# Kernel tuning notes

Hardware: AMD Instinct MI355X
Metric: run time of the kernel (lower is better)

Reference implementation:

```python
import jax, jax.numpy as jnp
import numpy as np

B, S, HID = 2, 2048, 2048
H, KVH, D = 32, 8, 64          # query heads, kv heads, head_dim
G = H // KVH                    # GQA group size (num_key_value_groups)
ROT = 32                        # head_dim * partial_rotary_factor
THETA = 10000.0
NEG = -1e9


def setup_inputs() -> dict:
    key = jax.random.key(0)
    ks = jax.random.split(key, 5)
    hidden_states = jax.random.normal(ks[0], (B, S, HID), jnp.float32) * 0.02
    Wq = jax.random.normal(ks[1], (H * D, HID), jnp.float32) * 0.02
    Wk = jax.random.normal(ks[2], (KVH * D, HID), jnp.float32) * 0.02
    Wv = jax.random.normal(ks[3], (KVH * D, HID), jnp.float32) * 0.02
    Wo = jax.random.normal(ks[4], (HID, H * D), jnp.float32) * 0.02
    # rotary embeddings over the partial rotary dims
    inv_freq = 1.0 / (THETA ** (jnp.arange(0, ROT, 2, dtype=jnp.float32) / ROT))
    freqs = jnp.arange(S, dtype=jnp.float32)[:, None] * inv_freq[None, :]  # [S, ROT/2]
    emb = jnp.concatenate([freqs, freqs], axis=-1)                         # [S, ROT]
    cos = jnp.broadcast_to(jnp.cos(emb)[None], (B, S, ROT)).astype(jnp.float32)
    sin = jnp.broadcast_to(jnp.sin(emb)[None], (B, S, ROT)).astype(jnp.float32)
    # HF-style additive causal mask [1, 1, S, S]
    causal = jnp.tril(jnp.ones((S, S), dtype=bool))
    attention_mask = jnp.where(causal, 0.0, NEG).astype(jnp.float32)[None, None]
    return {"hidden_states": hidden_states, "cos": cos, "sin": sin,
            "attention_mask": attention_mask, "Wq": Wq, "Wk": Wk, "Wv": Wv, "Wo": Wo}


def _rotate_half(x):
    half = x.shape[-1] // 2
    return jnp.concatenate([-x[..., half:], x[..., :half]], axis=-1)


def _apply_partial_rope(x, cos, sin):
    # x: [B, h, S, D]; cos/sin: [B, 1, S, ROT]
    xr, xp = x[..., :ROT], x[..., ROT:]
    xr = xr * cos + _rotate_half(xr) * sin
    return jnp.concatenate([xr, xp], axis=-1)


def reference(hidden_states, cos, sin, attention_mask, Wq, Wk, Wv, Wo):
    bsz, q_len, _ = hidden_states.shape
    q = (hidden_states @ Wq.T).reshape(bsz, q_len, H, D).transpose(0, 2, 1, 3)    # [B,H,S,D]
    k = (hidden_states @ Wk.T).reshape(bsz, q_len, KVH, D).transpose(0, 2, 1, 3)  # [B,KVH,S,D]
    v = (hidden_states @ Wv.T).reshape(bsz, q_len, KVH, D).transpose(0, 2, 1, 3)
    cos_e, sin_e = cos[:, None], sin[:, None]  # unsqueeze_dim=1
    q = _apply_partial_rope(q, cos_e, sin_e)
    k = _apply_partial_rope(k, cos_e, sin_e)
    # GQA: group q heads instead of materializing repeat_kv (same math)
    qg = q.reshape(bsz, KVH, G, q_len, D)
    scores = jnp.einsum('bkgsd,bktd->bkgst', qg, k) / jnp.sqrt(jnp.float32(D))
    scores = scores + attention_mask[:, :, None, :, :q_len]  # [B,KVH,G,S,S]
    attn = jax.nn.softmax(scores.astype(jnp.float32), axis=-1).astype(q.dtype)
    out = jnp.einsum('bkgst,bktd->bkgsd', attn, v)
    out = out.reshape(bsz, H, q_len, D).transpose(0, 2, 1, 3).reshape(bsz, q_len, H * D)
    return out @ Wo.T
```

## Files before the change

### kernel.cpp

```cpp
#include <hip/hip_runtime.h>
#include <hip/hip_bf16.h>

#define BATCH 2
#define SEQ 2048
#define HID 2048
#define NH 32
#define NKVH 8
#define HD 64
#define GQ 4
#define ROT 32

typedef __attribute__((ext_vector_type(8))) short bf16x8;
typedef __attribute__((ext_vector_type(8))) unsigned short u16x8;
typedef __attribute__((ext_vector_type(4))) float f32x4;
typedef unsigned int u32;
typedef unsigned short u16;

#define MFMA_BF16(A, B, C) __builtin_amdgcn_mfma_f32_16x16x32_bf16(A, B, C, 0, 0, 0)

#define QSCALE 0.180336880111120f

__device__ __forceinline__ void gload_lds16(const void* g, void* l) {
    __builtin_amdgcn_global_load_lds(
        (const __attribute__((address_space(1))) unsigned int*)g,
        (__attribute__((address_space(3))) unsigned int*)l, 16, 0, 0);
}

__device__ __forceinline__ u16 f2b(float x) {
    union { __hip_bfloat16 h; u16 u; } cv;
    cv.h = __float2bfloat16(x);
    return cv.u;
}
__device__ __forceinline__ u32 pack2r(float lo, float hi) {
    u32 a = __builtin_bit_cast(u32, lo) + 0x8000u;
    u32 b = __builtin_bit_cast(u32, hi) + 0x8000u;
    return __builtin_amdgcn_perm(b, a, 0x07060302u);
}

__global__ __launch_bounds__(256) void cast_all(
    const float* __restrict__ hs, const float* __restrict__ Wq,
    const float* __restrict__ Wk, const float* __restrict__ Wv,
    const float* __restrict__ Wo, u16* __restrict__ d_hs, u16* __restrict__ d_Wq,
    u16* __restrict__ d_Wk, u16* __restrict__ d_Wv, u16* __restrict__ d_Wo) {
    const int bx = blockIdx.x;
    const float* s;
    u16* d;
    int off;
    if (bx < 4096) { s = hs; d = d_hs; off = bx; }
    else if (bx < 6144) { s = Wq; d = d_Wq; off = bx - 4096; }
    else if (bx < 6656) { s = Wk; d = d_Wk; off = bx - 6144; }
    else if (bx < 7168) { s = Wv; d = d_Wv; off = bx - 6656; }
    else { s = Wo; d = d_Wo; off = bx - 7168; }
    const size_t i = (size_t)off * 2048 + threadIdx.x * 8;
    const float4 a = *(const float4*)&s[i];
    const float4 b = *(const float4*)&s[i + 4];
    u16x8 v;
    v[0] = f2b(a.x); v[1] = f2b(a.y); v[2] = f2b(a.z); v[3] = f2b(a.w);
    v[4] = f2b(b.x); v[5] = f2b(b.y); v[6] = f2b(b.z); v[7] = f2b(b.w);
    *(u16x8*)&d[i] = v;
}

__global__ __launch_bounds__(256) void qkv_gemm(
    const u16* __restrict__ A, const u16* __restrict__ Wq,
    const u16* __restrict__ Wk, const u16* __restrict__ Wv,
    u16* __restrict__ Qb, u16* __restrict__ Kb, u16* __restrict__ Vt,
    const float* __restrict__ cosp, const float* __restrict__ sinp) {
    const int bid = blockIdx.x;
    const int xcd = bid & 7, loc = bid >> 3;
    const int x = xcd * 3 + (loc % 3);
    const int m0 = (loc / 3) * 128;

    int mode, n0;
    const u16* __restrict__ W;
    if (x < 16)      { mode = 0; W = Wq; n0 = x * 128; }
    else if (x < 20) { mode = 1; W = Wk; n0 = (x - 16) * 128; }
    else             { mode = 2; W = Wv; n0 = (x - 20) * 128; }

    __shared__ __align__(16) u16 As[128 * 64];
    __shared__ __align__(16) u16 Ws[128 * 64];
    const int tid = threadIdx.x;
    const int lane = tid & 63, wave = tid >> 6;
    const int ar = lane & 15, quad = lane >> 4;
    const int q4 = quad * 4;
    const int wm = (wave >> 1) * 64, wn = (wave & 1) * 64;

    f32x4 acc[4][4] = {};

    for (int k0 = 0; k0 < HID; k0 += 64) {
#pragma unroll
        for (int it = 0; it < 4; ++it) {
            const int ci = it * 256 + tid;
            const int row = ci >> 3, kcl = ci & 7;
            const int kcg = kcl ^ (row & 7);
            gload_lds16(&A[(size_t)(m0 + row) * HID + k0 + kcg * 8], &As[ci * 8]);
            gload_lds16(&W[(size_t)(n0 + row) * HID + k0 + kcg * 8], &Ws[ci * 8]);
        }
        __syncthreads();
#pragma unroll
        for (int kh = 0; kh < 2; ++kh) {
            bf16x8 af[4], bf[4];
#pragma unroll
            for (int t = 0; t < 4; ++t) {
                const int ra = wm + t * 16 + ar;
                af[t] = *(const bf16x8*)&As[ra * 64 + (((kh * 4 + quad) ^ (ra & 7))) * 8];
                const int rb = wn + t * 16 + ar;
                bf[t] = *(const bf16x8*)&Ws[rb * 64 + (((kh * 4 + quad) ^ (rb & 7))) * 8];
            }
            if (mode < 2) {
#pragma unroll
                for (int mt = 0; mt < 4; ++mt)
#pragma unroll
                    for (int nt = 0; nt < 4; ++nt)
                        acc[mt][nt] = MFMA_BF16(bf[nt], af[mt], acc[mt][nt]);
            } else {
#pragma unroll
                for (int mt = 0; mt < 4; ++mt)
#pragma unroll
                    for (int nt = 0; nt < 4; ++nt)
                        acc[mt][nt] = MFMA_BF16(af[mt], bf[nt], acc[mt][nt]);
            }
        }
        __syncthreads();
    }

    if (mode < 2) {
        const float SC = (mode == 0) ? QSCALE : 1.0f;
        u16* __restrict__ C = (mode == 0) ? Qb : Kb;
        const int N = (mode == 0) ? 2048 : 512;
#pragma unroll
        for (int mt = 0; mt < 4; ++mt) {
            const int t = m0 + wm + mt * 16 + ar;
            const float4 c0 = *(const float4*)&cosp[(size_t)t * ROT + q4];
            const float4 s0 = *(const float4*)&sinp[(size_t)t * ROT + q4];
            const float4 c1 = *(const float4*)&cosp[(size_t)t * ROT + 16 + q4];
            const float4 s1 = *(const float4*)&sinp[(size_t)t * ROT + 16 + q4];
            u16* crow = &C[(size_t)t * N + n0 + wn];
            const f32x4 x0 = acc[mt][0], x1 = acc[mt][1];
            const float cr0[4] = {c0.x, c0.y, c0.z, c0.w};
            const float sr0[4] = {s0.x, s0.y, s0.z, s0.w};
            const float cr1[4] = {c1.x, c1.y, c1.z, c1.w};
            const float sr1[4] = {s1.x, s1.y, s1.z, s1.w};
            float o0[4], o1[4];
#pragma unroll
            for (int r = 0; r < 4; ++r) {
                o0[r] = (x0[r] * cr0[r] - x1[r] * sr0[r]) * SC;
                o1[r] = (x1[r] * cr1[r] + x0[r] * sr1[r]) * SC;
            }
            uint2 v;
            v.x = pack2r(o0[0], o0[1]); v.y = pack2r(o0[2], o0[3]);
            *(uint2*)&crow[q4] = v;
            v.x = pack2r(o1[0], o1[1]); v.y = pack2r(o1[2], o1[3]);
            *(uint2*)&crow[16 + q4] = v;
            v.x = pack2r(acc[mt][2][0] * SC, acc[mt][2][1] * SC);
            v.y = pack2r(acc[mt][2][2] * SC, acc[mt][2][3] * SC);
            *(uint2*)&crow[32 + q4] = v;
            v.x = pack2r(acc[mt][3][0] * SC, acc[mt][3][1] * SC);
            v.y = pack2r(acc[mt][3][2] * SC, acc[mt][3][3] * SC);
            *(uint2*)&crow[48 + q4] = v;
        }
    } else {
#pragma unroll
        for (int mt = 0; mt < 4; ++mt) {
            const int r0 = m0 + wm + mt * 16 + q4;
            const int bb = r0 >> 11;
            const int s = r0 & 2047;
            const int ca = (s >> 2) & 7;
            const int cl = ((ca & 3) << 1) | (ca >> 2);
            const int spos = (s & ~31) + cl * 4;
#pragma unroll
            for (int nt = 0; nt < 4; ++nt) {
                const int c = n0 + wn + nt * 16 + ar;
                const int kvh = c >> 6, d = c & 63;
                uint2 v;
                v.x = pack2r(acc[mt][nt][0], acc[mt][nt][1]);
                v.y = pack2r(acc[mt][nt][2], acc[mt][nt][3]);
                *(uint2*)&Vt[((size_t)(bb * NKVH + kvh) * HD + d) * SEQ + spos] = v;
            }
        }
    }
}

__global__ __launch_bounds__(256) void gemm_bt(const u16* __restrict__ A,
                                               const u16* __restrict__ W,
                                               float* __restrict__ C,
                                               int M, int N, int K) {
    const int bid = blockIdx.x;
    const int xcd = bid & 7, loc = bid >> 3;
    const int n0 = (xcd * 2 + (loc & 1)) * 128;
    const int m0 = (loc >> 1) * 128;

    __shared__ __align__(16) u16 As[128 * 64];
    __shared__ __align__(16) u16 Ws[128 * 64];
    const int tid = threadIdx.x;
    const int lane = tid & 63, wave = tid >> 6;
    const int ar = lane & 15, quad = lane >> 4;
    const int q4 = quad * 4;
    const int wm = (wave >> 1) * 64, wn = (wave & 1) * 64;

    f32x4 acc[4][4] = {};

    for (int k0 = 0; k0 < K; k0 += 64) {
#pragma unroll
        for (int it = 0; it < 4; ++it) {
            const int ci = it * 256 + tid;
            const int row = ci >> 3, kcl = ci & 7;
            const int kcg = kcl ^ (row & 7);
            gload_lds16(&A[(size_t)(m0 + row) * K + k0 + kcg * 8], &As[ci * 8]);
            gload_lds16(&W[(size_t)(n0 + row) * K + k0 + kcg * 8], &Ws[ci * 8]);
        }
        __syncthreads();
#pragma unroll
        for (int kh = 0; kh < 2; ++kh) {
            bf16x8 af[4], bf[4];
#pragma unroll
            for (int t = 0; t < 4; ++t) {
                const int ra = wm + t * 16 + ar;
                af[t] = *(const bf16x8*)&As[ra * 64 + (((kh * 4 + quad) ^ (ra & 7))) * 8];
                const int rb = wn + t * 16 + ar;
                bf[t] = *(const bf16x8*)&Ws[rb * 64 + (((kh * 4 + quad) ^ (rb & 7))) * 8];
            }
#pragma unroll
            for (int mt = 0; mt < 4; ++mt)
#pragma unroll
                for (int nt = 0; nt < 4; ++nt)
                    acc[mt][nt] = MFMA_BF16(bf[nt], af[mt], acc[mt][nt]);
        }
        __syncthreads();
    }

#pragma unroll
    for (int mt = 0; mt < 4; ++mt) {
        const int t = m0 + wm + mt * 16 + ar;
#pragma unroll
        for (int nt = 0; nt < 4; ++nt) {
            float4 v = {acc[mt][nt][0], acc[mt][nt][1], acc[mt][nt][2], acc[mt][nt][3]};
            *(float4*)&C[(size_t)t * N + n0 + wn + nt * 16 + q4] = v;
        }
    }
}

__global__ __launch_bounds__(256, 2) void flash_attn_mfma(
    const u16* __restrict__ Qg, const u16* __restrict__ Kg,
    const u16* __restrict__ Vtg, u16* __restrict__ AO) {
    const int p = blockIdx.x, h = blockIdx.y, b = blockIdx.z;
    const int kvh = h / GQ;
    const int tid = threadIdx.x;
    const int lane = tid & 63, w = tid >> 6;
    const int n = lane & 15, quad = lane >> 4;

    __shared__ __align__(16) u16 Qs[128 * 64];
    __shared__ __align__(16) u16 Ks[2 * 64 * 64];
    __shared__ __align__(16) u16 Vts[2 * 64 * 64];

    for (int ph = 0; ph < 2; ++ph) {
        const int bq = ph ? (15 - p) : p;
        const int q0 = bq * 128;

#pragma unroll
        for (int it = 0; it < 4; ++it) {
            const int ci = it * 256 + tid;
            const int row = ci >> 3, kcg = (ci & 7) ^ (row & 7);
            gload_lds16(&Qg[(size_t)((b * SEQ + q0 + row) * NH + h) * HD + kcg * 8],
                        &Qs[ci * 8]);
        }
#pragma unroll
        for (int it = 0; it < 2; ++it) {
            const int ci = it * 256 + tid;
            const int row = ci >> 3, kcg = (ci & 7) ^ (row & 7);
            gload_lds16(&Kg[(size_t)((b * SEQ + row) * NKVH + kvh) * HD + kcg * 8],
                        &Ks[ci * 8]);
            gload_lds16(&Vtg[(size_t)((b * NKVH + kvh) * HD + row) * SEQ + kcg * 8],
                        &Vts[ci * 8]);
        }
        __syncthreads();

        bf16x8 Qf[2][2];
#pragma unroll
        for (int t = 0; t < 2; ++t)
#pragma unroll
            for (int kh = 0; kh < 2; ++kh) {
                const int qrow = w * 32 + t * 16 + n;
                const int c = (kh * 4 + quad) ^ (qrow & 7);
                Qf[t][kh] = *(const bf16x8*)&Qs[qrow * 64 + c * 8];
            }

        f32x4 O[2][4] = {};
        float lsum[2] = {0.f, 0.f};

        const int ktmax = 2 * bq + 1;
        for (int kt = 0; kt <= ktmax; ++kt) {
            const int cur = kt & 1;
            if (kt < ktmax) {
                const int base = (cur ^ 1) * 4096;
#pragma unroll
                for (int it = 0; it < 2; ++it) {
                    const int ci = it * 256 + tid;
                    const int row = ci >> 3, kcg = (ci & 7) ^ (row & 7);
                    gload_lds16(&Kg[(size_t)((b * SEQ + (kt + 1) * 64 + row) * NKVH + kvh) * HD + kcg * 8],
                                &Ks[base + ci * 8]);
                    gload_lds16(&Vtg[(size_t)((b * NKVH + kvh) * HD + row) * SEQ + (kt + 1) * 64 + kcg * 8],
                                &Vts[base + ci * 8]);
                }
            }
            const u16* Kl = &Ks[cur * 4096];
            const u16* Vl = &Vts[cur * 4096];

            f32x4 sc[2][4] = {};
#pragma unroll
            for (int kh = 0; kh < 2; ++kh)
#pragma unroll
                for (int k4 = 0; k4 < 4; ++k4) {
                    const int krow = k4 * 16 + n;
                    const int c = (kh * 4 + quad) ^ (krow & 7);
                    const bf16x8 Kf = *(const bf16x8*)&Kl[krow * 64 + c * 8];
                    sc[0][k4] = MFMA_BF16(Kf, Qf[0][kh], sc[0][k4]);
                    sc[1][k4] = MFMA_BF16(Kf, Qf[1][kh], sc[1][k4]);
                }

            const bool masked = (kt >= 2 * bq);
            bf16x8 Pf[2][2];
#pragma unroll
            for (int t = 0; t < 2; ++t) {
                const int qg = q0 + w * 32 + t * 16 + n;
                if (masked) {
#pragma unroll
                    for (int k4 = 0; k4 < 4; ++k4)
#pragma unroll
                        for (int r = 0; r < 4; ++r)
                            if (kt * 64 + k4 * 16 + quad * 4 + r > qg)
                                sc[t][k4][r] = -1e30f;
                }
                float sk[4];
#pragma unroll
                for (int k4 = 0; k4 < 4; ++k4) {
                    const float e0 = exp2f(sc[t][k4][0]);
                    const float e1 = exp2f(sc[t][k4][1]);
                    const float e2 = exp2f(sc[t][k4][2]);
                    const float e3 = exp2f(sc[t][k4][3]);
                    sc[t][k4][0] = e0; sc[t][k4][1] = e1;
                    sc[t][k4][2] = e2; sc[t][k4][3] = e3;
                    sk[k4] = (e0 + e1) + (e2 + e3);
                }
                lsum[t] += (sk[0] + sk[1]) + (sk[2] + sk[3]);
#pragma unroll
                for (int kb = 0; kb < 2; ++kb) {
                    union { u32 uw[4]; bf16x8 v; } cv;
#pragma unroll
                    for (int a = 0; a < 2; ++a) {
                        cv.uw[a * 2 + 0] = pack2r(sc[t][2 * kb + a][0], sc[t][2 * kb + a][1]);
                        cv.uw[a * 2 + 1] = pack2r(sc[t][2 * kb + a][2], sc[t][2 * kb + a][3]);
                    }
                    Pf[t][kb] = cv.v;
                }
            }

#pragma unroll
            for (int kb = 0; kb < 2; ++kb)
#pragma unroll
                for (int dt = 0; dt < 4; ++dt) {
                    const int drow = dt * 16 + n;
                    const int c = (kb * 4 + quad) ^ (drow & 7);
                    const bf16x8 Vf = *(const bf16x8*)&Vl[drow * 64 + c * 8];
                    O[0][dt] = MFMA_BF16(Vf, Pf[0][kb], O[0][dt]);
                    O[1][dt] = MFMA_BF16(Vf, Pf[1][kb], O[1][dt]);
                }
            __syncthreads();
        }

#pragma unroll
        for (int t = 0; t < 2; ++t) {
            float rs = lsum[t];
            rs += __shfl_xor(rs, 16, 64);
            rs += __shfl_xor(rs, 32, 64);
            const int qg = q0 + w * 32 + t * 16 + n;
            const float inv = 1.f / rs;
#pragma unroll
            for (int dt = 0; dt < 4; ++dt) {
                uint2 v2;
                v2.x = pack2r(O[t][dt][0] * inv, O[t][dt][1] * inv);
                v2.y = pack2r(O[t][dt][2] * inv, O[t][dt][3] * inv);
                *(uint2*)&AO[(size_t)((b * SEQ + qg) * NH + h) * HD + dt * 16 + quad * 4] = v2;
            }
        }
    }
}

extern "C" void kernel_launch(void* const* d_in, const int* in_sizes, int n_in,
                              void* d_out, int out_size, void* d_ws,
                              size_t ws_size, hipStream_t stream) {
    const float* hs = (const float*)d_in[0];
    const float* cosp = (const float*)d_in[1];
    const float* sinp = (const float*)d_in[2];
    const float* Wq = (const float*)d_in[4];
    const float* Wk = (const float*)d_in[5];
    const float* Wv = (const float*)d_in[6];
    const float* Wo = (const float*)d_in[7];
    float* out = (float*)d_out;

    u16* ws = (u16*)d_ws;
    u16* hs_bf = ws;
    u16* Wq_bf = hs_bf + (size_t)4096 * 2048;
    u16* Wk_bf = Wq_bf + (size_t)2048 * 2048;
    u16* Wv_bf = Wk_bf + (size_t)512 * 2048;
    u16* Wo_bf = Wv_bf + (size_t)512 * 2048;
    u16* Qb = Wo_bf + (size_t)2048 * 2048;
    u16* Kb = Qb + (size_t)4096 * 2048;
    u16* Vt = Kb + (size_t)4096 * 512;
    u16* AO = hs_bf;

    cast_all<<<dim3(9216), 256, 0, stream>>>(hs, Wq, Wk, Wv, Wo, hs_bf, Wq_bf,
                                             Wk_bf, Wv_bf, Wo_bf);

    qkv_gemm<<<dim3(768), 256, 0, stream>>>(hs_bf, Wq_bf, Wk_bf, Wv_bf, Qb,
                                            Kb, Vt, cosp, sinp);

    flash_attn_mfma<<<dim3(8, NH, BATCH), 256, 0, stream>>>(Qb, Kb, Vt, AO);

    gemm_bt<<<dim3(512), 256, 0, stream>>>(AO, Wo_bf, out, 4096, 2048, 2048);
}
```

Before: 308.2 us.

## Rewrite QKV GEMM as 256x256 tile with double-buffered async LDS pipeline

The fused QKV projection GEMM now uses 512-thread blocks that each compute a 256x256 output tile, with 128KB of dynamic LDS. Global-to-LDS loads for iteration t+2 are interleaved with the MFMA phases of iteration t across two buffers, using explicit vmcnt waits, barriers and s_setprio. The goal is to raise data reuse per block and hide load latency behind matrix math. In exchange there are only 192 blocks, fewer than the CU count, a larger accumulator register footprint, and many barriers per k-step.

```diff
diff --git a/kernel.cpp b/kernel.cpp
--- a/kernel.cpp
+++ b/kernel.cpp
@@ -60,82 +60,139 @@
     *(u16x8*)&d[i] = v;
 }
 
-__global__ __launch_bounds__(256) void qkv_gemm(
+__global__ __launch_bounds__(512) void qkv_gemm(
     const u16* __restrict__ A, const u16* __restrict__ Wq,
     const u16* __restrict__ Wk, const u16* __restrict__ Wv,
     u16* __restrict__ Qb, u16* __restrict__ Kb, u16* __restrict__ Vt,
     const float* __restrict__ cosp, const float* __restrict__ sinp) {
+    extern __shared__ __align__(16) u16 lds[];
+    u16* Asl = lds;
+    u16* Wsl = lds + 32768;
+
     const int bid = blockIdx.x;
-    const int xcd = bid & 7, loc = bid >> 3;
-    const int x = xcd * 3 + (loc % 3);
-    const int m0 = (loc / 3) * 128;
+    const int wg = (bid & 7) * 24 + (bid >> 3);
+    const int mt = wg / 12, nt = wg % 12;
+    const int m0 = mt * 256;
 
     int mode, n0;
     const u16* __restrict__ W;
-    if (x < 16)      { mode = 0; W = Wq; n0 = x * 128; }
-    else if (x < 20) { mode = 1; W = Wk; n0 = (x - 16) * 128; }
-    else             { mode = 2; W = Wv; n0 = (x - 20) * 128; }
-
-    __shared__ __align__(16) u16 As[128 * 64];
-    __shared__ __align__(16) u16 Ws[128 * 64];
+    if (nt < 8)       { mode = 0; W = Wq; n0 = nt * 256; }
+    else if (nt < 10) { mode = 1; W = Wk; n0 = (nt - 8) * 256; }
+    else              { mode = 2; W = Wv; n0 = (nt - 10) * 256; }
+
     const int tid = threadIdx.x;
-    const int lane = tid & 63, wave = tid >> 6;
-    const int ar = lane & 15, quad = lane >> 4;
-    const int q4 = quad * 4;
-    const int wm = (wave >> 1) * 64, wn = (wave & 1) * 64;
-
-    f32x4 acc[4][4] = {};
-
-    for (int k0 = 0; k0 < HID; k0 += 64) {
-#pragma unroll
-        for (int it = 0; it < 4; ++it) {
-            const int ci = it * 256 + tid;
-            const int row = ci >> 3, kcl = ci & 7;
-            const int kcg = kcl ^ (row & 7);
-            gload_lds16(&A[(size_t)(m0 + row) * HID + k0 + kcg * 8], &As[ci * 8]);
-            gload_lds16(&W[(size_t)(n0 + row) * HID + k0 + kcg * 8], &Ws[ci * 8]);
-        }
-        __syncthreads();
-#pragma unroll
-        for (int kh = 0; kh < 2; ++kh) {
-            bf16x8 af[4], bf[4];
-#pragma unroll
-            for (int t = 0; t < 4; ++t) {
-                const int ra = wm + t * 16 + ar;
-                af[t] = *(const bf16x8*)&As[ra * 64 + (((kh * 4 + quad) ^ (ra & 7))) * 8];
-                const int rb = wn + t * 16 + ar;
-                bf[t] = *(const bf16x8*)&Ws[rb * 64 + (((kh * 4 + quad) ^ (rb & 7))) * 8];
-            }
-            if (mode < 2) {
-#pragma unroll
-                for (int mt = 0; mt < 4; ++mt)
-#pragma unroll
-                    for (int nt = 0; nt < 4; ++nt)
-                        acc[mt][nt] = MFMA_BF16(bf[nt], af[mt], acc[mt][nt]);
-            } else {
-#pragma unroll
-                for (int mt = 0; mt < 4; ++mt)
-#pragma unroll
-                    for (int nt = 0; nt < 4; ++nt)
-                        acc[mt][nt] = MFMA_BF16(af[mt], bf[nt], acc[mt][nt]);
-            }
-        }
-        __syncthreads();
-    }
+    const int lane = tid & 63, w = tid >> 6;
+    const int wr = w >> 2, wc = w & 3;
+    const int ar = lane & 15, quad = lane >> 4, q4 = quad * 4;
+
+    f32x4 acc[8][4] = {};
+    bf16x8 af[4][2], wf0[2][2], wf1[2][2];
+
+#define STAGE_A_Q(b, h, c, tt) { \
+    const int ci_ = (c) * 512 + tid; \
+    const int row_ = ci_ >> 3, kcg_ = (ci_ & 7) ^ (row_ & 7); \
+    gload_lds16(&A[(size_t)(m0 + (h) * 128 + row_) * HID + (tt) * 64 + kcg_ * 8], \
+                &Asl[((b) * 2 + (h)) * 8192 + ci_ * 8]); }
+#define STAGE_W_Q(b, h, c, tt) { \
+    const int ci_ = (c) * 512 + tid; \
+    const int row_ = ci_ >> 3, kcg_ = (ci_ & 7) ^ (row_ & 7); \
+    gload_lds16(&W[(size_t)(n0 + (h) * 128 + row_) * HID + (tt) * 64 + kcg_ * 8], \
+                &Wsl[((b) * 2 + (h)) * 8192 + ci_ * 8]); }
+#define LDA_F(dst, mj, kh) { \
+    const int r_ = (mj) * 16 + ar; \
+    dst = *(const bf16x8*)&Asl[(cur * 2 + wr) * 8192 + r_ * 64 + \
+                               ((((kh) * 4 + quad) ^ (r_ & 7)) * 8)]; }
+#define LDW_F(dst, nj, kh) { \
+    const int r_ = (wc & 1) * 64 + (nj) * 16 + ar; \
+    dst = *(const bf16x8*)&Wsl[(cur * 2 + (wc >> 1)) * 8192 + r_ * 64 + \
+                               ((((kh) * 4 + quad) ^ (r_ & 7)) * 8)]; }
+#define MFMA_QUAD(mh, nh, WF) \
+    if (mode < 2) { \
+        _Pragma("unroll") for (int kh = 0; kh < 2; ++kh) \
+        _Pragma("unroll") for (int mi = 0; mi < 4; ++mi) \
+        _Pragma("unroll") for (int ni = 0; ni < 2; ++ni) \
+            acc[(mh) * 4 + mi][(nh) * 2 + ni] = \
+                MFMA_BF16(WF[ni][kh], af[mi][kh], acc[(mh) * 4 + mi][(nh) * 2 + ni]); \
+    } else { \
+        _Pragma("unroll") for (int kh = 0; kh < 2; ++kh) \
+        _Pragma("unroll") for (int mi = 0; mi < 4; ++mi) \
+        _Pragma("unroll") for (int ni = 0; ni < 2; ++ni) \
+            acc[(mh) * 4 + mi][(nh) * 2 + ni] = \
+                MFMA_BF16(af[mi][kh], WF[ni][kh], acc[(mh) * 4 + mi][(nh) * 2 + ni]); \
+    }
+
+    STAGE_A_Q(0, 0, 0, 0); STAGE_A_Q(0, 0, 1, 0);
+    STAGE_A_Q(0, 1, 0, 0); STAGE_A_Q(0, 1, 1, 0);
+    STAGE_W_Q(0, 0, 0, 0); STAGE_W_Q(0, 0, 1, 0);
+    STAGE_W_Q(0, 1, 0, 0); STAGE_W_Q(0, 1, 1, 0);
+    STAGE_A_Q(1, 0, 0, 1); STAGE_A_Q(1, 0, 1, 1);
+    STAGE_A_Q(1, 1, 0, 1); STAGE_A_Q(1, 1, 1, 1);
+    STAGE_W_Q(1, 0, 0, 1); STAGE_W_Q(1, 0, 1, 1);
+    STAGE_W_Q(1, 1, 0, 1); STAGE_W_Q(1, 1, 1, 1);
+
+#pragma unroll 2
+    for (int t = 0; t < 32; ++t) {
+        const int cur = t & 1;
+        const int t2 = (t + 2 < 32) ? (t + 2) : 31;
+        asm volatile("s_waitcnt vmcnt(8)" ::: "memory");
+        __builtin_amdgcn_s_barrier();
+#pragma unroll
+        for (int mi = 0; mi < 4; ++mi) { LDA_F(af[mi][0], mi, 0); LDA_F(af[mi][1], mi, 1); }
+#pragma unroll
+        for (int ni = 0; ni < 2; ++ni) { LDW_F(wf0[ni][0], ni, 0); LDW_F(wf0[ni][1], ni, 1); }
+        __builtin_amdgcn_s_barrier();
+        asm volatile("s_waitcnt lgkmcnt(0)" ::: "memory");
+        __builtin_amdgcn_s_setprio(1);
+        MFMA_QUAD(0, 0, wf0);
+        __builtin_amdgcn_s_setprio(0);
+        __builtin_amdgcn_s_barrier();
+#pragma unroll
+        for (int ni = 0; ni < 2; ++ni) { LDW_F(wf1[ni][0], 2 + ni, 0); LDW_F(wf1[ni][1], 2 + ni, 1); }
+        STAGE_A_Q(cur, 0, 0, t2); STAGE_A_Q(cur, 1, 0, t2);
+        __builtin_amdgcn_s_barrier();
+        asm volatile("s_waitcnt lgkmcnt(0)" ::: "memory");
+        __builtin_amdgcn_s_setprio(1);
+        MFMA_QUAD(0, 1, wf1);
+        __builtin_amdgcn_s_setprio(0);
+        __builtin_amdgcn_s_barrier();
+#pragma unroll
+        for (int mi = 0; mi < 4; ++mi) { LDA_F(af[mi][0], 4 + mi, 0); LDA_F(af[mi][1], 4 + mi, 1); }
+        STAGE_W_Q(cur, 0, 0, t2); STAGE_W_Q(cur, 0, 1, t2);
+        __builtin_amdgcn_s_barrier();
+        asm volatile("s_waitcnt lgkmcnt(0)" ::: "memory");
+        __builtin_amdgcn_s_setprio(1);
+        MFMA_QUAD(1, 1, wf1);
+        __builtin_amdgcn_s_setprio(0);
+        __builtin_amdgcn_s_barrier();
+        STAGE_A_Q(cur, 0, 1, t2); STAGE_A_Q(cur, 1, 1, t2);
+        STAGE_W_Q(cur, 1, 0, t2); STAGE_W_Q(cur, 1, 1, t2);
+        __builtin_amdgcn_s_barrier();
+        __builtin_amdgcn_s_setprio(1);
+        MFMA_QUAD(1, 0, wf0);
+        __builtin_amdgcn_s_setprio(0);
+        __builtin_amdgcn_s_barrier();
+    }
+    asm volatile("s_waitcnt vmcnt(0)" ::: "memory");
+
+#undef STAGE_A_Q
+#undef STAGE_W_Q
+#undef LDA_F
+#undef LDW_F
+#undef MFMA_QUAD
 
     if (mode < 2) {
         const float SC = (mode == 0) ? QSCALE : 1.0f;
         u16* __restrict__ C = (mode == 0) ? Qb : Kb;
         const int N = (mode == 0) ? 2048 : 512;
 #pragma unroll
-        for (int mt = 0; mt < 4; ++mt) {
-            const int t = m0 + wm + mt * 16 + ar;
+        for (int mi = 0; mi < 8; ++mi) {
+            const int t = m0 + wr * 128 + mi * 16 + ar;
             const float4 c0 = *(const float4*)&cosp[(size_t)t * ROT + q4];
             const float4 s0 = *(const float4*)&sinp[(size_t)t * ROT + q4];
             const float4 c1 = *(const float4*)&cosp[(size_t)t * ROT + 16 + q4];
             const float4 s1 = *(const float4*)&sinp[(size_t)t * ROT + 16 + q4];
-            u16* crow = &C[(size_t)t * N + n0 + wn];
-            const f32x4 x0 = acc[mt][0], x1 = acc[mt][1];
+            u16* crow = &C[(size_t)t * N + n0 + wc * 64];
+            const f32x4 x0 = acc[mi][0], x1 = acc[mi][1];
             const float cr0[4] = {c0.x, c0.y, c0.z, c0.w};
             const float sr0[4] = {s0.x, s0.y, s0.z, s0.w};
             const float cr1[4] = {c1.x, c1.y, c1.z, c1.w};
@@ -151,29 +208,29 @@
             *(uint2*)&crow[q4] = v;
             v.x = pack2r(o1[0], o1[1]); v.y = pack2r(o1[2], o1[3]);
             *(uint2*)&crow[16 + q4] = v;
-            v.x = pack2r(acc[mt][2][0] * SC, acc[mt][2][1] * SC);
-            v.y = pack2r(acc[mt][2][2] * SC, acc[mt][2][3] * SC);
+            v.x = pack2r(acc[mi][2][0] * SC, acc[mi][2][1] * SC);
+            v.y = pack2r(acc[mi][2][2] * SC, acc[mi][2][3] * SC);
             *(uint2*)&crow[32 + q4] = v;
-            v.x = pack2r(acc[mt][3][0] * SC, acc[mt][3][1] * SC);
-            v.y = pack2r(acc[mt][3][2] * SC, acc[mt][3][3] * SC);
+            v.x = pack2r(acc[mi][3][0] * SC, acc[mi][3][1] * SC);
+            v.y = pack2r(acc[mi][3][2] * SC, acc[mi][3][3] * SC);
             *(uint2*)&crow[48 + q4] = v;
         }
     } else {
 #pragma unroll
-        for (int mt = 0; mt < 4; ++mt) {
-            const int r0 = m0 + wm + mt * 16 + q4;
+        for (int mi = 0; mi < 8; ++mi) {
+            const int r0 = m0 + wr * 128 + mi * 16 + q4;
             const int bb = r0 >> 11;
             const int s = r0 & 2047;
             const int ca = (s >> 2) & 7;
             const int cl = ((ca & 3) << 1) | (ca >> 2);
             const int spos = (s & ~31) + cl * 4;
 #pragma unroll
-            for (int nt = 0; nt < 4; ++nt) {
-                const int c = n0 + wn + nt * 16 + ar;
+            for (int ni = 0; ni < 4; ++ni) {
+                const int c = n0 + wc * 64 + ni * 16 + ar;
                 const int kvh = c >> 6, d = c & 63;
                 uint2 v;
-                v.x = pack2r(acc[mt][nt][0], acc[mt][nt][1]);
-                v.y = pack2r(acc[mt][nt][2], acc[mt][nt][3]);
+                v.x = pack2r(acc[mi][ni][0], acc[mi][ni][1]);
+                v.y = pack2r(acc[mi][ni][2], acc[mi][ni][3]);
                 *(uint2*)&Vt[((size_t)(bb * NKVH + kvh) * HD + d) * SEQ + spos] = v;
             }
         }
@@ -408,11 +465,18 @@
     u16* Vt = Kb + (size_t)4096 * 512;
     u16* AO = hs_bf;
 
+    static bool attr_done = false;
+    if (!attr_done) {
+        hipFuncSetAttribute(reinterpret_cast<const void*>(qkv_gemm),
+                            hipFuncAttributeMaxDynamicSharedMemorySize, 131072);
+        attr_done = true;
+    }
+
     cast_all<<<dim3(9216), 256, 0, stream>>>(hs, Wq, Wk, Wv, Wo, hs_bf, Wq_bf,
                                              Wk_bf, Wv_bf, Wo_bf);
 
-    qkv_gemm<<<dim3(768), 256, 0, stream>>>(hs_bf, Wq_bf, Wk_bf, Wv_bf, Qb,
-                                            Kb, Vt, cosp, sinp);
+    qkv_gemm<<<dim3(192), 512, 131072, stream>>>(hs_bf, Wq_bf, Wk_bf, Wv_bf,
+                                                 Qb, Kb, Vt, cosp, sinp);
 
     flash_attn_mfma<<<dim3(8, NH, BATCH), 256, 0, stream>>>(Qb, Kb, Vt, AO);
 
```

Measured after the change: 413.8 us. 1.34x slower.
